# Optimization experiments

Measured on AMD Instinct MI355X. Metric: run time of the kernel, lower is better.

Reference implementation:

```python
import jax, jax.numpy as jnp
import numpy as np

H = 128          # image resolution (matches init_kwargs H)
B = 2            # batch (matches init_kwargs B)
F = 1024         # number of triangle faces
PI = 3.141592653589793


def setup_inputs() -> dict:
    key = jax.random.key(0)
    # vertices in NDC [-1, 1]: [B, faces, 3 verts, xyz]
    v = jax.random.uniform(key, (B, F, 3, 3), dtype=jnp.float32, minval=-1.0, maxval=1.0)
    return {"v_tensor": v, "C": 16}


def _render(tmp, C):
    # tmp: [B,F,3,3] with (x,y) already in pixel coords, z in [-1,1].
    # Counting-sort rasterization expressed in closed form: instead of sorting
    # per-pixel ray/mesh intersections into in/out intervals, we use the signed
    # (winding-number) formulation: occupancy f(zt) = sum_i s_i * H(zt - zt_i)
    # where s_i = +1 for front faces, -1 for back faces. The cosine (FOF)
    # coefficients then reduce to a sum over intersections -- fully vectorized.
    x = tmp[..., 0]  # [B,F,3]
    y = tmp[..., 1]
    z = tmp[..., 2]
    px = jnp.arange(H, dtype=tmp.dtype)[None, :]   # pixel-center x, [1,H]
    py = jnp.arange(H, dtype=tmp.dtype)[:, None]   # pixel-center y, [H,1]

    def vert(i):
        return x[..., i, None, None], y[..., i, None, None], z[..., i, None, None]

    x0, y0, z0 = vert(0)
    x1, y1, z1 = vert(1)
    x2, y2, z2 = vert(2)

    # edge functions -> barycentric numerators, each [B,F,H,H]
    e0 = (x2 - x1) * (py - y1) - (y2 - y1) * (px - x1)
    e1 = (x0 - x2) * (py - y2) - (y0 - y2) * (px - x2)
    e2 = (x1 - x0) * (py - y0) - (y1 - y0) * (px - x0)
    area = (x1 - x0) * (y2 - y0) - (x2 - x0) * (y1 - y0)  # [B,F,1,1]

    nz = area != 0
    inv = jnp.where(nz, 1.0 / jnp.where(nz, area, 1.0), 0.0)
    l0, l1, l2 = e0 * inv, e1 * inv, e2 * inv
    inside = (l0 >= 0) & (l1 >= 0) & (l2 >= 0) & nz
    s = jnp.sign(area)                      # front/back facing sign
    w = jnp.where(inside, s, jnp.zeros((), tmp.dtype))  # [B,F,H,H]

    # interpolated depth, remapped to zt in [0,1]
    zt = jnp.clip((l0 * z0 + l1 * z1 + l2 * z2 + 1.0) * 0.5, 0.0, 1.0)

    # Fourier occupancy coefficients over zt in [0,1]:
    #   c0 = int f dzt           = sum_i s_i * (1 - zt_i)
    #   ck = 2 int f cos(k pi zt) dzt = -2/(k pi) * sum_i s_i * sin(k pi zt_i)
    coeffs = [jnp.sum(w * (1.0 - zt), axis=1)]            # [B,H,H]
    for k in range(1, C):
        coeffs.append(jnp.sum(w * jnp.sin((k * PI) * zt), axis=1) * (-2.0 / (k * PI)))
    return jnp.stack(coeffs, axis=1)  # [B,C,H,H]


def reference(v_tensor, C):
    a = jnp.array([H / 2.0, -H / 2.0, 1.0], dtype=v_tensor.dtype)
    b = jnp.array([H / 2.0 - 0.5, H / 2.0 - 0.5, 0.0], dtype=v_tensor.dtype)
    tmp = v_tensor * a + b  # affine transform from the torch forward
    return _render(tmp, C)
```

## Files before the change

### kernel.cpp

```cpp
#include <hip/hip_runtime.h>
#include <math.h>

#define HH 128
#define BB 2
#define FF 1024
#define CC 16
#define PIF 3.14159265358979323846f

typedef float f2 __attribute__((ext_vector_type(2)));

__global__ __launch_bounds__(256) void fof_setup(const float* __restrict__ v,
                                                 float* __restrict__ recf,
                                                 double* __restrict__ recd,
                                                 int* __restrict__ bbox) {
    int idx = blockIdx.x * 256 + threadIdx.x;
    if (idx >= BB * FF) return;
    const float* vp = v + (size_t)idx * 9;

    double X0 = fma((double)vp[0],  64.0, 63.5);
    double Y0 = fma((double)vp[1], -64.0, 63.5);
    double Z0 = (double)vp[2];
    double X1 = fma((double)vp[3],  64.0, 63.5);
    double Y1 = fma((double)vp[4], -64.0, 63.5);
    double Z1 = (double)vp[5];
    double X2 = fma((double)vp[6],  64.0, 63.5);
    double Y2 = fma((double)vp[7], -64.0, 63.5);
    double Z2 = (double)vp[8];

    double d0x = X2 - X1, d0y = Y2 - Y1;
    double d1x = X0 - X2, d1y = Y0 - Y2;
    double d2x = X1 - X0, d2y = Y1 - Y0;
    double area = d1x * d2y - d1y * d2x;
    double inv  = (area != 0.0) ? 1.0 / area : 0.0;
    double sg   = (area > 0.0) ? 1.0 : ((area < 0.0) ? -1.0 : 0.0);

    double A0 = d0x * inv, B0 = -d0y * inv, C0 = (d0y * X1 - d0x * Y1) * inv;
    double A1 = d1x * inv, B1 = -d1y * inv, C1 = (d1y * X2 - d1x * Y2) * inv;
    double A2 = d2x * inv, B2 = -d2y * inv, C2 = (d2y * X0 - d2x * Y0) * inv;

    double ZA = (A0 * Z0 + A1 * Z1 + A2 * Z2) * 0.5;
    double ZB = (B0 * Z0 + B1 * Z1 + B2 * Z2) * 0.5;
    double ZC = (C0 * Z0 + C1 * Z1 + C2 * Z2 + 1.0) * 0.5;

    double M0 = (fabs(A0) + fabs(B0)) * 135.0 + fabs(C0);
    double M1 = (fabs(A1) + fabs(B1)) * 135.0 + fabs(C1);
    double M2 = (fabs(A2) + fabs(B2)) * 135.0 + fabs(C2);
    float eps = (float)(1e-6 * fmax(M0, fmax(M1, M2)));

    float* rf = recf + (size_t)idx * 16;
    rf[0] = (float)A0; rf[1] = (float)B0; rf[2] = (float)C0;
    rf[3] = (float)A1; rf[4] = (float)B1; rf[5] = (float)C1;
    rf[6] = (float)A2; rf[7] = (float)B2; rf[8] = (float)C2;
    rf[9] = (float)ZA; rf[10] = (float)ZB; rf[11] = (float)ZC;
    rf[12] = (float)sg; rf[13] = eps; rf[14] = 0.f; rf[15] = 0.f;

    double* rd = recd + (size_t)idx * 10;
    rd[0] = A0; rd[1] = B0; rd[2] = C0;
    rd[3] = A1; rd[4] = B1; rd[5] = C1;
    rd[6] = A2; rd[7] = B2; rd[8] = C2; rd[9] = 0.0;

    float x0 = (float)X0, y0 = (float)Y0;
    float x1 = (float)X1, y1 = (float)Y1;
    float x2 = (float)X2, y2 = (float)Y2;
    float xmn = fminf(x0, fminf(x1, x2)) - 0.5f;
    float xmx = fmaxf(x0, fmaxf(x1, x2)) + 0.5f;
    float ymn = fminf(y0, fminf(y1, y2)) - 0.5f;
    float ymx = fmaxf(y0, fmaxf(y1, y2)) + 0.5f;
    int txmin = (int)ceilf((xmn - 7.f) * 0.125f);
    int txmax = (int)floorf(xmx * 0.125f);
    int tymin = (int)ceilf((ymn - 7.f) * 0.125f);
    int tymax = (int)floorf(ymx * 0.125f);
    txmin = max(0, min(15, txmin)); txmax = max(0, min(15, txmax));
    tymin = max(0, min(15, tymin)); tymax = max(0, min(15, tymax));
    bbox[idx] = (sg == 0.0) ? (1 | (0 << 8) | (1 << 16) | (0 << 24))
                            : (txmin | (txmax << 8) | (tymin << 16) | (tymax << 24));
}

__global__ __launch_bounds__(1024) void fof_main(const float* __restrict__ recf,
                                                 const double* __restrict__ recd,
                                                 const int* __restrict__ bbox,
                                                 float* __restrict__ out) {
    __shared__ float S1[8][64][17];
    __shared__ float S2[4][64][17];
    __shared__ float S3[2][64][17];
    __shared__ float S4[64][17];

    int blk  = blockIdx.x;
    int b    = blk & 1;
    int t0   = blk >> 1;
    int tile = b ? (t0 ^ 0x88) : t0;
    int ty   = tile >> 4;
    int tx   = tile & 15;
    int wv   = __builtin_amdgcn_readfirstlane((int)(threadIdx.x >> 6));
    int lane = threadIdx.x & 63;

    float px = (float)(tx * 8 + (lane & 7));
    float py = (float)(ty * 8 + (lane >> 3));

    float acc0 = 0.f, acc15 = 0.f;
    f2 accP[7];
#pragma unroll
    for (int j = 0; j < 7; ++j) { accP[j].x = 0.f; accP[j].y = 0.f; }

    int gfb = b * FF + wv * 64;

    int pk = bbox[gfb + lane];
    int txmin = pk & 255, txmax = (pk >> 8) & 255;
    int tymin = (pk >> 16) & 255, tymax = (pk >> 24) & 255;
    bool pass = !((tx < txmin) | (tx > txmax) | (ty < tymin) | (ty > tymax));
    unsigned long long m = __ballot(pass);

    while (m) {
        int j = __builtin_ctzll(m);
        m &= m - 1;
        j = __builtin_amdgcn_readfirstlane(j);
        const float* r = recf + (size_t)(gfb + j) * 16;

        float l0 = fmaf(r[0], py, fmaf(r[1], px, r[2]));
        float l1 = fmaf(r[3], py, fmaf(r[4], px, r[5]));
        float l2 = fmaf(r[6], py, fmaf(r[7], px, r[8]));
        float eps = r[13];
        float lmin = fminf(fminf(l0, l1), l2);
        float amin = fminf(fminf(__builtin_fabsf(l0), __builtin_fabsf(l1)),
                           __builtin_fabsf(l2));
        bool inside = lmin >= 0.f;
        bool unc    = amin < eps;
        if (__builtin_expect(__any(unc), 0)) {
            const double* rd = recd + (size_t)(gfb + j) * 10;
            double pyd = (double)py, pxd = (double)px;
            double L0 = fma(rd[0], pyd, fma(rd[1], pxd, rd[2]));
            double L1 = fma(rd[3], pyd, fma(rd[4], pxd, rd[5]));
            double L2 = fma(rd[6], pyd, fma(rd[7], pxd, rd[8]));
            inside = (L0 >= 0.0) & (L1 >= 0.0) & (L2 >= 0.0);
        }
        float w = inside ? r[12] : 0.f;

        if (__any(w != 0.f)) {
            float zt = fmaf(r[9], py, fmaf(r[10], px, r[11]));
            zt = fminf(fmaxf(zt, 0.f), 1.f);
            float hz = 0.5f * zt;
            float s1, s2, c2;
            asm("v_sin_f32 %0, %1" : "=v"(s1) : "v"(hz));
            asm("v_sin_f32 %0, %1" : "=v"(s2) : "v"(zt));
            asm("v_cos_f32 %0, %1" : "=v"(c2) : "v"(zt));
            float twoc2 = c2 + c2;

            acc0 = fmaf(w, 1.f - zt, acc0);
            f2 w2;  w2.x = w;      w2.y = w;
            f2 t2;  t2.x = twoc2;  t2.y = twoc2;
            f2 um1; um1.x = -s1;   um1.y = 0.f;
            f2 u0;  u0.x = s1;     u0.y = s2;
            accP[0] += w2 * u0;
            f2 u1 = t2 * u0 - um1;  accP[1] += w2 * u1;
            f2 u2 = t2 * u1 - u0;   accP[2] += w2 * u2;
            f2 u3 = t2 * u2 - u1;   accP[3] += w2 * u3;
            f2 u4 = t2 * u3 - u2;   accP[4] += w2 * u4;
            f2 u5 = t2 * u4 - u3;   accP[5] += w2 * u5;
            f2 u6 = t2 * u5 - u4;   accP[6] += w2 * u6;
            float s15 = fmaf(twoc2, u6.x, -u5.x);
            acc15 = fmaf(w, s15, acc15);
        }
    }

    float accv[16];
    accv[0] = acc0;
#pragma unroll
    for (int j = 0; j < 7; ++j) { accv[2 * j + 1] = accP[j].x; accv[2 * j + 2] = accP[j].y; }
    accv[15] = acc15;

    if (wv >= 8) {
#pragma unroll
        for (int k = 0; k < CC; ++k) S1[wv - 8][lane][k] = accv[k];
    }
    __syncthreads();
    if (wv < 8) {
#pragma unroll
        for (int k = 0; k < CC; ++k) accv[k] += S1[wv][lane][k];
    }
    if (wv >= 4 && wv < 8) {
#pragma unroll
        for (int k = 0; k < CC; ++k) S2[wv - 4][lane][k] = accv[k];
    }
    __syncthreads();
    if (wv < 4) {
#pragma unroll
        for (int k = 0; k < CC; ++k) accv[k] += S2[wv][lane][k];
    }
    if (wv == 2 || wv == 3) {
#pragma unroll
        for (int k = 0; k < CC; ++k) S3[wv - 2][lane][k] = accv[k];
    }
    __syncthreads();
    if (wv < 2) {
#pragma unroll
        for (int k = 0; k < CC; ++k) accv[k] += S3[wv][lane][k];
    }
    if (wv == 1) {
#pragma unroll
        for (int k = 0; k < CC; ++k) S4[lane][k] = accv[k];
    }
    __syncthreads();
    if (wv == 0) {
        int xo = tx * 8 + (lane & 7);
        int yo = ty * 8 + (lane >> 3);
#pragma unroll
        for (int k = 0; k < CC; ++k) {
            float val = accv[k] + S4[lane][k];
            float scale = (k == 0) ? 1.f : (-2.f / (PIF * (float)k));
            out[(((b * CC + k) * HH) + yo) * HH + xo] = val * scale;
        }
    }
}

extern "C" void kernel_launch(void* const* d_in, const int* in_sizes, int n_in,
                              void* d_out, int out_size, void* d_ws, size_t ws_size,
                              hipStream_t stream) {
    const float* v = (const float*)d_in[0];
    float* out = (float*)d_out;

    float*  recf = (float*)d_ws;
    double* recd = (double*)((char*)d_ws + 131072);
    int*    bbox = (int*)((char*)d_ws + 131072 + 163840);

    fof_setup<<<(BB * FF + 255) / 256, 256, 0, stream>>>(v, recf, recd, bbox);
    fof_main<<<BB * 256, 1024, 0, stream>>>(recf, recd, bbox, out);
}
```

Baseline: 75.53 us.

## Split faces across two blocks with atomic output, prefetch next face record

Each tile now runs as two 512-thread blocks, each handling half the faces, so the grid doubles and the block-level reduction gets shorter. The two partial results are combined with atomicAdd into an output that is zeroed by an added memset. The face loop now software-pipelines the next face's coefficient loads while the current face is evaluated, and tiles are assigned to blocks with a swizzled order. The cost is an extra memset, atomics on every output element, and a nondeterministic summation order.

```diff
diff --git a/kernel.cpp b/kernel.cpp
--- a/kernel.cpp
+++ b/kernel.cpp
@@ -76,19 +76,21 @@
                             : (txmin | (txmax << 8) | (tymin << 16) | (tymax << 24));
 }
 
-__global__ __launch_bounds__(1024) void fof_main(const float* __restrict__ recf,
-                                                 const double* __restrict__ recd,
-                                                 const int* __restrict__ bbox,
-                                                 float* __restrict__ out) {
-    __shared__ float S1[8][64][17];
-    __shared__ float S2[4][64][17];
-    __shared__ float S3[2][64][17];
-    __shared__ float S4[64][17];
-
-    int blk  = blockIdx.x;
-    int b    = blk & 1;
-    int t0   = blk >> 1;
-    int tile = b ? (t0 ^ 0x88) : t0;
+__global__ __launch_bounds__(512) void fof_main(const float* __restrict__ recf,
+                                                const double* __restrict__ recd,
+                                                const int* __restrict__ bbox,
+                                                float* __restrict__ out) {
+    __shared__ float S1[4][64][17];
+    __shared__ float S2[2][64][17];
+    __shared__ float S3[64][17];
+
+    int i  = blockIdx.x;
+    int u  = i & 255;
+    int kb = i >> 8;
+    int u2 = ((u & 1) << 3) | ((u & 2) << 6) | ((u >> 2) & 7) | (((u >> 5) & 7) << 4);
+    int tile = u2 ^ (kb * 0x55);
+    int b    = kb & 1;
+    int half = kb >> 1;
     int ty   = tile >> 4;
     int tx   = tile & 15;
     int wv   = __builtin_amdgcn_readfirstlane((int)(threadIdx.x >> 6));
@@ -102,7 +104,7 @@
 #pragma unroll
     for (int j = 0; j < 7; ++j) { accP[j].x = 0.f; accP[j].y = 0.f; }
 
-    int gfb = b * FF + wv * 64;
+    int gfb = b * FF + half * 512 + wv * 64;
 
     int pk = bbox[gfb + lane];
     int txmin = pk & 255, txmax = (pk >> 8) & 255;
@@ -110,55 +112,78 @@
     bool pass = !((tx < txmin) | (tx > txmax) | (ty < tymin) | (ty > tymax));
     unsigned long long m = __ballot(pass);
 
-    while (m) {
-        int j = __builtin_ctzll(m);
+    if (m) {
+        int j = __builtin_amdgcn_readfirstlane(__builtin_ctzll(m));
         m &= m - 1;
-        j = __builtin_amdgcn_readfirstlane(j);
         const float* r = recf + (size_t)(gfb + j) * 16;
-
-        float l0 = fmaf(r[0], py, fmaf(r[1], px, r[2]));
-        float l1 = fmaf(r[3], py, fmaf(r[4], px, r[5]));
-        float l2 = fmaf(r[6], py, fmaf(r[7], px, r[8]));
-        float eps = r[13];
-        float lmin = fminf(fminf(l0, l1), l2);
-        float amin = fminf(fminf(__builtin_fabsf(l0), __builtin_fabsf(l1)),
-                           __builtin_fabsf(l2));
-        bool inside = lmin >= 0.f;
-        bool unc    = amin < eps;
-        if (__builtin_expect(__any(unc), 0)) {
-            const double* rd = recd + (size_t)(gfb + j) * 10;
-            double pyd = (double)py, pxd = (double)px;
-            double L0 = fma(rd[0], pyd, fma(rd[1], pxd, rd[2]));
-            double L1 = fma(rd[3], pyd, fma(rd[4], pxd, rd[5]));
-            double L2 = fma(rd[6], pyd, fma(rd[7], pxd, rd[8]));
-            inside = (L0 >= 0.0) & (L1 >= 0.0) & (L2 >= 0.0);
-        }
-        float w = inside ? r[12] : 0.f;
-
-        if (__any(w != 0.f)) {
-            float zt = fmaf(r[9], py, fmaf(r[10], px, r[11]));
-            zt = fminf(fmaxf(zt, 0.f), 1.f);
-            float hz = 0.5f * zt;
-            float s1, s2, c2;
-            asm("v_sin_f32 %0, %1" : "=v"(s1) : "v"(hz));
-            asm("v_sin_f32 %0, %1" : "=v"(s2) : "v"(zt));
-            asm("v_cos_f32 %0, %1" : "=v"(c2) : "v"(zt));
-            float twoc2 = c2 + c2;
-
-            acc0 = fmaf(w, 1.f - zt, acc0);
-            f2 w2;  w2.x = w;      w2.y = w;
-            f2 t2;  t2.x = twoc2;  t2.y = twoc2;
-            f2 um1; um1.x = -s1;   um1.y = 0.f;
-            f2 u0;  u0.x = s1;     u0.y = s2;
-            accP[0] += w2 * u0;
-            f2 u1 = t2 * u0 - um1;  accP[1] += w2 * u1;
-            f2 u2 = t2 * u1 - u0;   accP[2] += w2 * u2;
-            f2 u3 = t2 * u2 - u1;   accP[3] += w2 * u3;
-            f2 u4 = t2 * u3 - u2;   accP[4] += w2 * u4;
-            f2 u5 = t2 * u4 - u3;   accP[5] += w2 * u5;
-            f2 u6 = t2 * u5 - u4;   accP[6] += w2 * u6;
-            float s15 = fmaf(twoc2, u6.x, -u5.x);
-            acc15 = fmaf(w, s15, acc15);
+        float cA0 = r[0], cB0 = r[1], cC0 = r[2];
+        float cA1 = r[3], cB1 = r[4], cC1 = r[5];
+        float cA2 = r[6], cB2 = r[7], cC2 = r[8];
+        float cZA = r[9], cZB = r[10], cZC = r[11];
+        float cSg = r[12], cEps = r[13];
+
+        for (;;) {
+            bool hn = (m != 0);
+            unsigned long long msafe = m | (unsigned long long)(m == 0);
+            int jn = __builtin_amdgcn_readfirstlane(__builtin_ctzll(msafe));
+            m &= m - 1;
+            const float* rn = recf + (size_t)(gfb + jn) * 16;
+            float nA0 = rn[0], nB0 = rn[1], nC0 = rn[2];
+            float nA1 = rn[3], nB1 = rn[4], nC1 = rn[5];
+            float nA2 = rn[6], nB2 = rn[7], nC2 = rn[8];
+            float nZA = rn[9], nZB = rn[10], nZC = rn[11];
+            float nSg = rn[12], nEps = rn[13];
+
+            float l0 = fmaf(cA0, py, fmaf(cB0, px, cC0));
+            float l1 = fmaf(cA1, py, fmaf(cB1, px, cC1));
+            float l2 = fmaf(cA2, py, fmaf(cB2, px, cC2));
+            float lmin = fminf(fminf(l0, l1), l2);
+            float amin = fminf(fminf(__builtin_fabsf(l0), __builtin_fabsf(l1)),
+                               __builtin_fabsf(l2));
+            bool inside = lmin >= 0.f;
+            if (__builtin_expect(__any(amin < cEps), 0)) {
+                const double* rd = recd + (size_t)(gfb + j) * 10;
+                double pyd = (double)py, pxd = (double)px;
+                double L0 = fma(rd[0], pyd, fma(rd[1], pxd, rd[2]));
+                double L1 = fma(rd[3], pyd, fma(rd[4], pxd, rd[5]));
+                double L2 = fma(rd[6], pyd, fma(rd[7], pxd, rd[8]));
+                inside = (L0 >= 0.0) & (L1 >= 0.0) & (L2 >= 0.0);
+            }
+            float w = inside ? cSg : 0.f;
+
+            if (__any(w != 0.f)) {
+                float zt = fmaf(cZA, py, fmaf(cZB, px, cZC));
+                zt = fminf(fmaxf(zt, 0.f), 1.f);
+                float hz = 0.5f * zt;
+                float s1, s2, c2;
+                asm("v_sin_f32 %0, %1" : "=v"(s1) : "v"(hz));
+                asm("v_sin_f32 %0, %1" : "=v"(s2) : "v"(zt));
+                asm("v_cos_f32 %0, %1" : "=v"(c2) : "v"(zt));
+                float twoc2 = c2 + c2;
+
+                acc0 = fmaf(w, 1.f - zt, acc0);
+                f2 w2;  w2.x = w;      w2.y = w;
+                f2 t2;  t2.x = twoc2;  t2.y = twoc2;
+                f2 um1; um1.x = -s1;   um1.y = 0.f;
+                f2 u0;  u0.x = s1;     u0.y = s2;
+                accP[0] += w2 * u0;
+                f2 u1 = t2 * u0 - um1;  accP[1] += w2 * u1;
+                f2 uu2 = t2 * u1 - u0;  accP[2] += w2 * uu2;
+                f2 u3 = t2 * uu2 - u1;  accP[3] += w2 * u3;
+                f2 u4 = t2 * u3 - uu2;  accP[4] += w2 * u4;
+                f2 u5 = t2 * u4 - u3;   accP[5] += w2 * u5;
+                f2 u6 = t2 * u5 - u4;   accP[6] += w2 * u6;
+                float s15 = fmaf(twoc2, u6.x, -u5.x);
+                acc15 = fmaf(w, s15, acc15);
+            }
+
+            if (!hn) break;
+            j = jn;
+            cA0 = nA0; cB0 = nB0; cC0 = nC0;
+            cA1 = nA1; cB1 = nB1; cC1 = nC1;
+            cA2 = nA2; cB2 = nB2; cC2 = nC2;
+            cZA = nZA; cZB = nZB; cZC = nZC;
+            cSg = nSg; cEps = nEps;
         }
     }
 
@@ -168,36 +193,27 @@
     for (int j = 0; j < 7; ++j) { accv[2 * j + 1] = accP[j].x; accv[2 * j + 2] = accP[j].y; }
     accv[15] = acc15;
 
-    if (wv >= 8) {
-#pragma unroll
-        for (int k = 0; k < CC; ++k) S1[wv - 8][lane][k] = accv[k];
-    }
-    __syncthreads();
-    if (wv < 8) {
-#pragma unroll
-        for (int k = 0; k < CC; ++k) accv[k] += S1[wv][lane][k];
-    }
-    if (wv >= 4 && wv < 8) {
-#pragma unroll
-        for (int k = 0; k < CC; ++k) S2[wv - 4][lane][k] = accv[k];
+    if (wv >= 4) {
+#pragma unroll
+        for (int k = 0; k < CC; ++k) S1[wv - 4][lane][k] = accv[k];
     }
     __syncthreads();
     if (wv < 4) {
 #pragma unroll
-        for (int k = 0; k < CC; ++k) accv[k] += S2[wv][lane][k];
+        for (int k = 0; k < CC; ++k) accv[k] += S1[wv][lane][k];
     }
     if (wv == 2 || wv == 3) {
 #pragma unroll
-        for (int k = 0; k < CC; ++k) S3[wv - 2][lane][k] = accv[k];
+        for (int k = 0; k < CC; ++k) S2[wv - 2][lane][k] = accv[k];
     }
     __syncthreads();
     if (wv < 2) {
 #pragma unroll
-        for (int k = 0; k < CC; ++k) accv[k] += S3[wv][lane][k];
+        for (int k = 0; k < CC; ++k) accv[k] += S2[wv][lane][k];
     }
     if (wv == 1) {
 #pragma unroll
-        for (int k = 0; k < CC; ++k) S4[lane][k] = accv[k];
+        for (int k = 0; k < CC; ++k) S3[lane][k] = accv[k];
     }
     __syncthreads();
     if (wv == 0) {
@@ -205,9 +221,9 @@
         int yo = ty * 8 + (lane >> 3);
 #pragma unroll
         for (int k = 0; k < CC; ++k) {
-            float val = accv[k] + S4[lane][k];
+            float val = accv[k] + S3[lane][k];
             float scale = (k == 0) ? 1.f : (-2.f / (PIF * (float)k));
-            out[(((b * CC + k) * HH) + yo) * HH + xo] = val * scale;
+            atomicAdd(&out[(((b * CC + k) * HH) + yo) * HH + xo], val * scale);
         }
     }
 }
@@ -222,6 +238,7 @@
     double* recd = (double*)((char*)d_ws + 131072);
     int*    bbox = (int*)((char*)d_ws + 131072 + 163840);
 
+    hipMemsetAsync(d_out, 0, (size_t)out_size * sizeof(float), stream);
     fof_setup<<<(BB * FF + 255) / 256, 256, 0, stream>>>(v, recf, recd, bbox);
-    fof_main<<<BB * 256, 1024, 0, stream>>>(recf, recd, bbox, out);
+    fof_main<<<BB * 2 * 256, 512, 0, stream>>>(recf, recd, bbox, out);
 }
```

After: 78.38 us. 3.8% more time.

## Cull faces by exact tile edge test and process two faces per iteration

Applied to the files above, without the earlier changes.

Before the ballot, each lane evaluates its face's three edge functions at the tile corner that maximizes each one. Faces whose triangle cannot touch the 8x8 tile are dropped from the work mask, which tightens the bounding-box cull. The per-face loop is also unrolled to handle two faces per iteration through a shared inline body, with a liveness flag for an odd count, so loads and transcendentals can overlap. The dead second slot on odd counts still costs its loads and edge evaluation, and the eps margin keeps the cull conservative.

```diff
diff --git a/kernel.cpp b/kernel.cpp
--- a/kernel.cpp
+++ b/kernel.cpp
@@ -76,6 +76,54 @@
                             : (txmin | (txmax << 8) | (tymin << 16) | (tymax << 24));
 }
 
+__device__ __forceinline__ void fof_body(const float* __restrict__ r,
+                                         const double* __restrict__ rd,
+                                         bool live, float px, float py,
+                                         float& acc0, float& acc15, f2* accP) {
+    float l0 = fmaf(r[0], py, fmaf(r[1], px, r[2]));
+    float l1 = fmaf(r[3], py, fmaf(r[4], px, r[5]));
+    float l2 = fmaf(r[6], py, fmaf(r[7], px, r[8]));
+    float lmin = fminf(fminf(l0, l1), l2);
+    float amin = fminf(fminf(__builtin_fabsf(l0), __builtin_fabsf(l1)),
+                       __builtin_fabsf(l2));
+    bool inside = lmin >= 0.f;
+    if (__builtin_expect(live && __any(amin < r[13]), 0)) {
+        double pyd = (double)py, pxd = (double)px;
+        double L0 = fma(rd[0], pyd, fma(rd[1], pxd, rd[2]));
+        double L1 = fma(rd[3], pyd, fma(rd[4], pxd, rd[5]));
+        double L2 = fma(rd[6], pyd, fma(rd[7], pxd, rd[8]));
+        inside = (L0 >= 0.0) & (L1 >= 0.0) & (L2 >= 0.0);
+    }
+    float sg_eff = live ? r[12] : 0.f;
+    float w = inside ? sg_eff : 0.f;
+
+    if (__any(w != 0.f)) {
+        float zt = fmaf(r[9], py, fmaf(r[10], px, r[11]));
+        zt = fminf(fmaxf(zt, 0.f), 1.f);
+        float hz = 0.5f * zt;
+        float s1, s2, c2;
+        asm("v_sin_f32 %0, %1" : "=v"(s1) : "v"(hz));
+        asm("v_sin_f32 %0, %1" : "=v"(s2) : "v"(zt));
+        asm("v_cos_f32 %0, %1" : "=v"(c2) : "v"(zt));
+        float twoc2 = c2 + c2;
+
+        acc0 = fmaf(w, 1.f - zt, acc0);
+        f2 w2;  w2.x = w;      w2.y = w;
+        f2 t2;  t2.x = twoc2;  t2.y = twoc2;
+        f2 um1; um1.x = -s1;   um1.y = 0.f;
+        f2 u0;  u0.x = s1;     u0.y = s2;
+        accP[0] += w2 * u0;
+        f2 u1 = t2 * u0 - um1;  accP[1] += w2 * u1;
+        f2 uu2 = t2 * u1 - u0;  accP[2] += w2 * uu2;
+        f2 u3 = t2 * uu2 - u1;  accP[3] += w2 * u3;
+        f2 u4 = t2 * u3 - uu2;  accP[4] += w2 * u4;
+        f2 u5 = t2 * u4 - u3;   accP[5] += w2 * u5;
+        f2 u6 = t2 * u5 - u4;   accP[6] += w2 * u6;
+        float s15 = fmaf(twoc2, u6.x, -u5.x);
+        acc15 = fmaf(w, s15, acc15);
+    }
+}
+
 __global__ __launch_bounds__(1024) void fof_main(const float* __restrict__ recf,
                                                  const double* __restrict__ recd,
                                                  const int* __restrict__ bbox,
@@ -108,58 +156,41 @@
     int txmin = pk & 255, txmax = (pk >> 8) & 255;
     int tymin = (pk >> 16) & 255, tymax = (pk >> 24) & 255;
     bool pass = !((tx < txmin) | (tx > txmax) | (ty < tymin) | (ty > tymax));
+
+    {
+        const float* rl = recf + (size_t)(gfb + lane) * 16;
+        float4 q0 = *(const float4*)(rl);
+        float4 q1 = *(const float4*)(rl + 4);
+        float4 q2 = *(const float4*)(rl + 8);
+        float4 q3 = *(const float4*)(rl + 12);
+        float fx0 = (float)(tx * 8), fx1 = (float)(tx * 8 + 7);
+        float fy0 = (float)(ty * 8), fy1 = (float)(ty * 8 + 7);
+        float e0 = fmaf(q0.x, (q0.x >= 0.f ? fy1 : fy0),
+                   fmaf(q0.y, (q0.y >= 0.f ? fx1 : fx0), q0.z));
+        float e1 = fmaf(q0.w, (q0.w >= 0.f ? fy1 : fy0),
+                   fmaf(q1.x, (q1.x >= 0.f ? fx1 : fx0), q1.y));
+        float e2 = fmaf(q1.z, (q1.z >= 0.f ? fy1 : fy0),
+                   fmaf(q1.w, (q1.w >= 0.f ? fx1 : fx0), q2.x));
+        float eps = q3.y;
+        pass = pass & (e0 >= -eps) & (e1 >= -eps) & (e2 >= -eps);
+    }
     unsigned long long m = __ballot(pass);
 
     while (m) {
-        int j = __builtin_ctzll(m);
+        int j0 = __builtin_amdgcn_readfirstlane(__builtin_ctzll(m));
         m &= m - 1;
-        j = __builtin_amdgcn_readfirstlane(j);
-        const float* r = recf + (size_t)(gfb + j) * 16;
-
-        float l0 = fmaf(r[0], py, fmaf(r[1], px, r[2]));
-        float l1 = fmaf(r[3], py, fmaf(r[4], px, r[5]));
-        float l2 = fmaf(r[6], py, fmaf(r[7], px, r[8]));
-        float eps = r[13];
-        float lmin = fminf(fminf(l0, l1), l2);
-        float amin = fminf(fminf(__builtin_fabsf(l0), __builtin_fabsf(l1)),
-                           __builtin_fabsf(l2));
-        bool inside = lmin >= 0.f;
-        bool unc    = amin < eps;
-        if (__builtin_expect(__any(unc), 0)) {
-            const double* rd = recd + (size_t)(gfb + j) * 10;
-            double pyd = (double)py, pxd = (double)px;
-            double L0 = fma(rd[0], pyd, fma(rd[1], pxd, rd[2]));
-            double L1 = fma(rd[3], pyd, fma(rd[4], pxd, rd[5]));
-            double L2 = fma(rd[6], pyd, fma(rd[7], pxd, rd[8]));
-            inside = (L0 >= 0.0) & (L1 >= 0.0) & (L2 >= 0.0);
-        }
-        float w = inside ? r[12] : 0.f;
-
-        if (__any(w != 0.f)) {
-            float zt = fmaf(r[9], py, fmaf(r[10], px, r[11]));
-            zt = fminf(fmaxf(zt, 0.f), 1.f);
-            float hz = 0.5f * zt;
-            float s1, s2, c2;
-            asm("v_sin_f32 %0, %1" : "=v"(s1) : "v"(hz));
-            asm("v_sin_f32 %0, %1" : "=v"(s2) : "v"(zt));
-            asm("v_cos_f32 %0, %1" : "=v"(c2) : "v"(zt));
-            float twoc2 = c2 + c2;
-
-            acc0 = fmaf(w, 1.f - zt, acc0);
-            f2 w2;  w2.x = w;      w2.y = w;
-            f2 t2;  t2.x = twoc2;  t2.y = twoc2;
-            f2 um1; um1.x = -s1;   um1.y = 0.f;
-            f2 u0;  u0.x = s1;     u0.y = s2;
-            accP[0] += w2 * u0;
-            f2 u1 = t2 * u0 - um1;  accP[1] += w2 * u1;
-            f2 u2 = t2 * u1 - u0;   accP[2] += w2 * u2;
-            f2 u3 = t2 * u2 - u1;   accP[3] += w2 * u3;
-            f2 u4 = t2 * u3 - u2;   accP[4] += w2 * u4;
-            f2 u5 = t2 * u4 - u3;   accP[5] += w2 * u5;
-            f2 u6 = t2 * u5 - u4;   accP[6] += w2 * u6;
-            float s15 = fmaf(twoc2, u6.x, -u5.x);
-            acc15 = fmaf(w, s15, acc15);
-        }
+        bool have2 = (m != 0ULL);
+        unsigned long long ms = m | (unsigned long long)(m == 0ULL);
+        int j1 = __builtin_amdgcn_readfirstlane(__builtin_ctzll(ms));
+        m &= m - 1;
+
+        const float*  ra  = recf + (size_t)(gfb + j0) * 16;
+        const double* rda = recd + (size_t)(gfb + j0) * 10;
+        const float*  rb  = recf + (size_t)(gfb + j1) * 16;
+        const double* rdb = recd + (size_t)(gfb + j1) * 10;
+
+        fof_body(ra, rda, true,  px, py, acc0, acc15, accP);
+        fof_body(rb, rdb, have2, px, py, acc0, acc15, accP);
     }
 
     float accv[16];
```

New measurement: 74.33 us. Within noise of the previous version (-1.6%).
